# Kernel optimization log

Hardware: AMD Instinct MI355X
Metric: run time of the kernel (lower is better)

Reference implementation:

```python
import jax, jax.numpy as jnp
import numpy as np

B, T, C = 8, 2048, 1024
FFN = 4 * C
EPS = 1e-5


def layer_norm(x, scale, bias):
    mean = jnp.mean(x, axis=-1, keepdims=True)
    var = jnp.mean(jnp.square(x - mean), axis=-1, keepdims=True)
    return (x - mean) * jax.lax.rsqrt(var + EPS) * scale + bias


def token_shift(x):
    # prepend a zero timestep (zero initial state), drop last: x[:, t-1]
    return jnp.pad(x[:, :-1, :], ((0, 0), (1, 0), (0, 0)))


def wkv_scan(k, v, time_first, time_decay):
    # k, v: [B, T, C]. Numerically-stabilized RWKV WKV recurrence (TimeMixCell).
    w = -jnp.exp(time_decay)  # [C]

    def step(carry, kv):
        a, b, p = carry
        kt, vt = kv
        uk = kt + time_first
        q = jnp.maximum(p, uk)
        e1 = jnp.exp(p - q)
        e2 = jnp.exp(uk - q)
        num = e1 * a + e2 * vt
        den = e1 * b + e2
        wkv = jnp.where(den == 0, 0.0, num / jnp.where(den == 0, 1.0, den))
        cw = w + p
        q2 = jnp.maximum(cw, kt)
        f1 = jnp.exp(cw - q2)
        f2 = jnp.exp(kt - q2)
        return (f1 * a + f2 * vt, f1 * b + f2, q2), wkv

    a0 = jnp.zeros((B, C), dtype=k.dtype)
    b0 = jnp.zeros((B, C), dtype=k.dtype)
    p0 = jnp.full((B, C), 1.0 - 1e30, dtype=k.dtype)
    kT = jnp.moveaxis(k, 1, 0)  # [T, B, C]
    vT = jnp.moveaxis(v, 1, 0)
    _, wkvT = jax.lax.scan(step, (a0, b0, p0), (kT, vT))
    return jnp.moveaxis(wkvT, 0, 1)  # [B, T, C]


def setup_inputs() -> dict:
    key = jax.random.key(0)
    ks = jax.random.split(key, 20)
    n = lambda i, shape, s=1.0: jax.random.normal(ks[i], shape, dtype=jnp.float32) * s
    u = lambda i, shape: jax.random.uniform(ks[i], shape, dtype=jnp.float32)
    return {
        'x': n(0, (B, T, C)),
        'ln1_w': 1.0 + n(1, (C,), 0.02), 'ln1_b': n(2, (C,), 0.02),
        'tm_k': u(3, (C,)), 'tm_v': u(4, (C,)), 'tm_r': u(5, (C,)),
        'Wk': n(6, (C, C), 0.02), 'Wv': n(7, (C, C), 0.02), 'Wr': n(8, (C, C), 0.02),
        'time_first': n(9, (C,), 0.1), 'time_decay': n(10, (C,), 0.5),
        'Wo': n(11, (C, C), 0.02),
        'ln2_w': 1.0 + n(12, (C,), 0.02), 'ln2_b': n(13, (C,), 0.02),
        'cm_k': u(14, (C,)), 'cm_r': u(15, (C,)),
        'Wk_ffn': n(16, (C, FFN), 0.02), 'Wv_ffn': n(17, (FFN, C), 0.02),
        'Wr_ffn': n(18, (C, C), 0.02),
    }


def reference(x, ln1_w, ln1_b, tm_k, tm_v, tm_r, Wk, Wv, Wr, time_first,
              time_decay, Wo, ln2_w, ln2_b, cm_k, cm_r, Wk_ffn, Wv_ffn, Wr_ffn):
    # ---- TimeMixFirst ----
    xn = layer_norm(x, ln1_w, ln1_b)
    xs = token_shift(xn)
    kx = xn * tm_k + xs * (1.0 - tm_k)
    vx = xn * tm_v + xs * (1.0 - tm_v)
    rx = xn * tm_r + xs * (1.0 - tm_r)
    r = jax.nn.sigmoid(rx @ Wr)
    k = kx @ Wk
    v = vx @ Wv
    # ---- TimeMixCell (WKV recurrence) ----
    wkv = wkv_scan(k, v, time_first, time_decay)
    # ---- TimeMixLast ----
    att_out = x + (r * wkv) @ Wo
    # ---- ChannelMix ----
    yn = layer_norm(att_out, ln2_w, ln2_b)
    ys = token_shift(yn)
    kx2 = yn * cm_k + ys * (1.0 - cm_k)
    rx2 = yn * cm_r + ys * (1.0 - cm_r)
    r2 = jax.nn.sigmoid(rx2 @ Wr_ffn)
    vv = jnp.square(jax.nn.relu(kx2 @ Wk_ffn))
    return att_out + r2 * (vv @ Wv_ffn)
```

## Files before the change

kernel.cpp:

```cpp
#include <hip/hip_runtime.h>
#include <hip/hip_bf16.h>

#define B_   8
#define T_   2048
#define C_   1024
#define FFN_ 4096
#define M_   (B_ * T_)
#define EPS_ 1e-5f

typedef __bf16 bf16x8 __attribute__((ext_vector_type(8)));
typedef float  f32x4  __attribute__((ext_vector_type(4)));

__device__ __forceinline__ unsigned short f2bf(float f) {
    union { float f; unsigned int u; } c; c.f = f;
    unsigned int u = c.u;
    u += 0x7fffu + ((u >> 16) & 1u);
    return (unsigned short)(u >> 16);
}
__device__ __forceinline__ float bf2f(unsigned short h) {
    union { unsigned int u; float f; } c; c.u = ((unsigned int)h) << 16;
    return c.f;
}

__global__ __launch_bounds__(256) void wconv_t(const float* __restrict__ src,
                                               unsigned short* __restrict__ dst,
                                               int R, int Cc) {
    __shared__ float tile[32][33];
    int tx = threadIdx.x, ty = threadIdx.y;
    int c0 = blockIdx.x * 32;
    int r0 = blockIdx.y * 32;
#pragma unroll
    for (int i = 0; i < 4; ++i)
        tile[ty + i * 8][tx] = src[(size_t)(r0 + ty + i * 8) * Cc + c0 + tx];
    __syncthreads();
#pragma unroll
    for (int i = 0; i < 4; ++i)
        dst[(size_t)(c0 + ty + i * 8) * R + r0 + tx] = f2bf(tile[tx][ty + i * 8]);
}

__device__ __forceinline__ void block_stats(const float4* __restrict__ p4, int tid,
                                            float* red, float& mean, float& rstd) {
    float4 v = p4[tid];
    float s = v.x + v.y + v.z + v.w;
    float q = v.x * v.x + v.y * v.y + v.z * v.z + v.w * v.w;
#pragma unroll
    for (int off = 32; off >= 1; off >>= 1) {
        s += __shfl_down(s, off, 64);
        q += __shfl_down(q, off, 64);
    }
    int lane = tid & 63, wv = tid >> 6;
    if (lane == 0) { red[wv] = s; red[4 + wv] = q; }
    __syncthreads();
    s = red[0] + red[1] + red[2] + red[3];
    q = red[4] + red[5] + red[6] + red[7];
    mean = s * (1.0f / C_);
    float var = q * (1.0f / C_) - mean * mean;
    rstd = rsqrtf(var + EPS_);
    __syncthreads();
}

__global__ __launch_bounds__(256) void mix1_kernel(
    const float* __restrict__ x, const float* __restrict__ lnw, const float* __restrict__ lnb,
    const float* __restrict__ tmk, const float* __restrict__ tmv, const float* __restrict__ tmr,
    unsigned short* __restrict__ kx, unsigned short* __restrict__ vx, unsigned short* __restrict__ rx) {
    __shared__ float red[8];
    int token = blockIdx.x;
    int t = token & (T_ - 1);
    int tid = threadIdx.x;
    bool hp = (t != 0);
    const float4* xt = (const float4*)(x + (size_t)token * C_);
    const float4* xp = (const float4*)(x + (size_t)(hp ? token - 1 : token) * C_);
    float m1, r1, m0 = 0.f, r0 = 0.f;
    block_stats(xt, tid, red, m1, r1);
    if (hp) block_stats(xp, tid, red, m0, r0);

    float4 xv = xt[tid];
    float4 pv = xp[tid];
    float4 w4 = ((const float4*)lnw)[tid];
    float4 b4 = ((const float4*)lnb)[tid];
    float4 k4 = ((const float4*)tmk)[tid];
    float4 v4 = ((const float4*)tmv)[tid];
    float4 q4 = ((const float4*)tmr)[tid];

    ushort4 ko, vo, ro;
    auto mixone = [&](float xe, float pe, float we, float be, float ke, float ve, float re,
                      unsigned short& koe, unsigned short& voe, unsigned short& roe) {
        float xn = (xe - m1) * r1 * we + be;
        float xs = hp ? ((pe - m0) * r0 * we + be) : 0.f;
        koe = f2bf(xs + ke * (xn - xs));
        voe = f2bf(xs + ve * (xn - xs));
        roe = f2bf(xs + re * (xn - xs));
    };
    mixone(xv.x, pv.x, w4.x, b4.x, k4.x, v4.x, q4.x, ko.x, vo.x, ro.x);
    mixone(xv.y, pv.y, w4.y, b4.y, k4.y, v4.y, q4.y, ko.y, vo.y, ro.y);
    mixone(xv.z, pv.z, w4.z, b4.z, k4.z, v4.z, q4.z, ko.z, vo.z, ro.z);
    mixone(xv.w, pv.w, w4.w, b4.w, k4.w, v4.w, q4.w, ko.w, vo.w, ro.w);
    size_t o = (size_t)token * (C_ / 4) + tid;
    ((ushort4*)kx)[o] = ko;
    ((ushort4*)vx)[o] = vo;
    ((ushort4*)rx)[o] = ro;
}

__global__ __launch_bounds__(256) void mix2_kernel(
    const float* __restrict__ att, const float* __restrict__ lnw, const float* __restrict__ lnb,
    const float* __restrict__ cmk, const float* __restrict__ cmr,
    unsigned short* __restrict__ kx, unsigned short* __restrict__ rx) {
    __shared__ float red[8];
    int token = blockIdx.x;
    int t = token & (T_ - 1);
    int tid = threadIdx.x;
    bool hp = (t != 0);
    const float4* xt = (const float4*)(att + (size_t)token * C_);
    const float4* xp = (const float4*)(att + (size_t)(hp ? token - 1 : token) * C_);
    float m1, r1, m0 = 0.f, r0 = 0.f;
    block_stats(xt, tid, red, m1, r1);
    if (hp) block_stats(xp, tid, red, m0, r0);

    float4 xv = xt[tid];
    float4 pv = xp[tid];
    float4 w4 = ((const float4*)lnw)[tid];
    float4 b4 = ((const float4*)lnb)[tid];
    float4 k4 = ((const float4*)cmk)[tid];
    float4 q4 = ((const float4*)cmr)[tid];

    ushort4 ko, ro;
    auto mixone = [&](float xe, float pe, float we, float be, float ke, float re,
                      unsigned short& koe, unsigned short& roe) {
        float xn = (xe - m1) * r1 * we + be;
        float xs = hp ? ((pe - m0) * r0 * we + be) : 0.f;
        koe = f2bf(xs + ke * (xn - xs));
        roe = f2bf(xs + re * (xn - xs));
    };
    mixone(xv.x, pv.x, w4.x, b4.x, k4.x, q4.x, ko.x, ro.x);
    mixone(xv.y, pv.y, w4.y, b4.y, k4.y, q4.y, ko.y, ro.y);
    mixone(xv.z, pv.z, w4.z, b4.z, k4.z, q4.z, ko.z, ro.z);
    mixone(xv.w, pv.w, w4.w, b4.w, k4.w, q4.w, ko.w, ro.w);
    size_t o = (size_t)token * (C_ / 4) + tid;
    ((ushort4*)kx)[o] = ko;
    ((ushort4*)rx)[o] = ro;
}

__global__ __launch_bounds__(64) void wkv_scan_kernel(
    const float* __restrict__ k, const unsigned short* __restrict__ v,
    unsigned short* rv,
    const float* __restrict__ tf, const float* __restrict__ td) {
    int idx = blockIdx.x * 64 + threadIdx.x;
    int b = idx >> 10, c = idx & (C_ - 1);
    float w = -expf(td[c]);
    float u = tf[c];
    size_t base = (size_t)b * T_ * C_ + c;
    float a = 0.f, bb = 0.f, p = -1e30f;

    float kA[8], vA[8], rA[8], kB[8], vB[8], rB[8];
#pragma unroll
    for (int j = 0; j < 8; ++j) {
        size_t o = base + (size_t)j * C_;
        kA[j] = k[o]; vA[j] = bf2f(v[o]); rA[j] = bf2f(rv[o]);
    }

    auto step = [&](float kt, float vt, float rt, int t) {
        float uk = u + kt;
        float qq = fmaxf(p, uk);
        float e1 = __expf(p - qq), e2 = __expf(uk - qq);
        float num = e1 * a + e2 * vt;
        float den = e1 * bb + e2;
        float wkv = (den == 0.f) ? 0.f : num / den;
        rv[base + (size_t)t * C_] = f2bf(rt * wkv);
        float cw = w + p;
        float q2 = fmaxf(cw, kt);
        float f1 = __expf(cw - q2), f2e = __expf(kt - q2);
        a = f1 * a + f2e * vt;
        bb = f1 * bb + f2e;
        p = q2;
    };

    for (int t0 = 0; t0 < T_; t0 += 16) {
#pragma unroll
        for (int j = 0; j < 8; ++j) {
            int t = t0 + 8 + j; if (t > T_ - 1) t = T_ - 1;
            size_t o = base + (size_t)t * C_;
            kB[j] = k[o]; vB[j] = bf2f(v[o]); rB[j] = bf2f(rv[o]);
        }
#pragma unroll
        for (int j = 0; j < 8; ++j) step(kA[j], vA[j], rA[j], t0 + j);
#pragma unroll
        for (int j = 0; j < 8; ++j) {
            int t = t0 + 16 + j; if (t > T_ - 1) t = T_ - 1;
            size_t o = base + (size_t)t * C_;
            kA[j] = k[o]; vA[j] = bf2f(v[o]); rA[j] = bf2f(rv[o]);
        }
#pragma unroll
        for (int j = 0; j < 8; ++j) step(kB[j], vB[j], rB[j], t0 + 8 + j);
    }
}

template<int EPI>
__global__ __launch_bounds__(256) void gemm_bt(
    const unsigned short* __restrict__ A, const unsigned short* __restrict__ Bt,
    float* Cf, unsigned short* Cb,
    const float* __restrict__ e0f, const unsigned short* __restrict__ e0b,
    int M, int N, int K, int ldb) {
    __shared__ unsigned short Als[128 * 32];
    __shared__ unsigned short Bls[128 * 32];
    int tid = threadIdx.x;
    int lane = tid & 63, wv = tid >> 6;
    int wr = wv >> 1, wc = wv & 1;
    int brow = blockIdx.y * 128, bcol = blockIdx.x * 128;

    f32x4 acc[4][4] = {};

    int ar = tid >> 2, ac = (tid & 3) * 8;
    const unsigned short* ga0 = A + (size_t)(brow + ar) * K + ac;
    const unsigned short* ga1 = A + (size_t)(brow + 64 + ar) * K + ac;
    const unsigned short* gb0 = Bt + (size_t)(bcol + ar) * ldb + ac;
    const unsigned short* gb1 = Bt + (size_t)(bcol + 64 + ar) * ldb + ac;
    unsigned short* la0 = Als + (size_t)(wv * 64) * 8;
    unsigned short* la1 = Als + (size_t)((4 + wv) * 64) * 8;
    unsigned short* lb0 = Bls + (size_t)(wv * 64) * 8;
    unsigned short* lb1 = Bls + (size_t)((4 + wv) * 64) * 8;

    int fa = (lane & 15) * 32 + (lane >> 4) * 8;

    for (int kt = 0; kt < K; kt += 32) {
        __builtin_amdgcn_global_load_lds((const __attribute__((address_space(1))) void*)(ga0 + kt),
                                         (__attribute__((address_space(3))) void*)la0, 16, 0, 0);
        __builtin_amdgcn_global_load_lds((const __attribute__((address_space(1))) void*)(ga1 + kt),
                                         (__attribute__((address_space(3))) void*)la1, 16, 0, 0);
        __builtin_amdgcn_global_load_lds((const __attribute__((address_space(1))) void*)(gb0 + kt),
                                         (__attribute__((address_space(3))) void*)lb0, 16, 0, 0);
        __builtin_amdgcn_global_load_lds((const __attribute__((address_space(1))) void*)(gb1 + kt),
                                         (__attribute__((address_space(3))) void*)lb1, 16, 0, 0);
        __syncthreads();
        bf16x8 af[4], bfr[4];
#pragma unroll
        for (int m = 0; m < 4; ++m)
            af[m] = *(const bf16x8*)&Als[(wr * 64 + m * 16) * 32 + fa];
#pragma unroll
        for (int n = 0; n < 4; ++n)
            bfr[n] = *(const bf16x8*)&Bls[(wc * 64 + n * 16) * 32 + fa];
#pragma unroll
        for (int m = 0; m < 4; ++m)
#pragma unroll
            for (int n = 0; n < 4; ++n)
                acc[m][n] = __builtin_amdgcn_mfma_f32_16x16x32_bf16(af[m], bfr[n], acc[m][n], 0, 0, 0);
        __syncthreads();
    }

#pragma unroll
    for (int m = 0; m < 4; ++m) {
#pragma unroll
        for (int n = 0; n < 4; ++n) {
#pragma unroll
            for (int j = 0; j < 4; ++j) {
                int row = brow + wr * 64 + m * 16 + (lane >> 4) * 4 + j;
                int col = bcol + wc * 64 + n * 16 + (lane & 15);
                size_t o = (size_t)row * N + col;
                float val = acc[m][n][j];
                if constexpr (EPI == 0) Cf[o] = val;
                else if constexpr (EPI == 2) Cf[o] = val + e0f[o];
                else if constexpr (EPI == 3) { float tt = fmaxf(val, 0.f); Cb[o] = f2bf(tt * tt); }
                else if constexpr (EPI == 5) Cb[o] = f2bf(1.f / (1.f + __expf(-val)));
                else if constexpr (EPI == 6) Cb[o] = f2bf(val);
                else if constexpr (EPI == 7) Cf[o] = Cf[o] + bf2f(e0b[o]) * val;
            }
        }
    }
}

extern "C" void kernel_launch(void* const* d_in, const int* in_sizes, int n_in,
                              void* d_out, int out_size, void* d_ws, size_t ws_size,
                              hipStream_t stream) {
    const float* x    = (const float*)d_in[0];
    const float* ln1w = (const float*)d_in[1];
    const float* ln1b = (const float*)d_in[2];
    const float* tmk  = (const float*)d_in[3];
    const float* tmv  = (const float*)d_in[4];
    const float* tmr  = (const float*)d_in[5];
    const float* Wk   = (const float*)d_in[6];
    const float* Wv   = (const float*)d_in[7];
    const float* Wr   = (const float*)d_in[8];
    const float* tf   = (const float*)d_in[9];
    const float* td   = (const float*)d_in[10];
    const float* Wo   = (const float*)d_in[11];
    const float* ln2w = (const float*)d_in[12];
    const float* ln2b = (const float*)d_in[13];
    const float* cmk  = (const float*)d_in[14];
    const float* cmr  = (const float*)d_in[15];
    const float* Wkf  = (const float*)d_in[16];
    const float* Wvf  = (const float*)d_in[17];
    const float* Wrf  = (const float*)d_in[18];
    float* out = (float*)d_out;

    char* ws = (char*)d_ws;
    size_t off = 0;
    auto alloc = [&](size_t bytes) {
        char* p = ws + off;
        off += (bytes + 255) & ~(size_t)255;
        return p;
    };
    unsigned short* WkT  = (unsigned short*)alloc((size_t)C_ * C_ * 2);
    unsigned short* WvT  = (unsigned short*)alloc((size_t)C_ * C_ * 2);
    unsigned short* WrT  = (unsigned short*)alloc((size_t)C_ * C_ * 2);
    unsigned short* WoT  = (unsigned short*)alloc((size_t)C_ * C_ * 2);
    unsigned short* WrfT = (unsigned short*)alloc((size_t)C_ * C_ * 2);
    unsigned short* WkfT = (unsigned short*)alloc((size_t)C_ * FFN_ * 2);
    unsigned short* WvfT = (unsigned short*)alloc((size_t)FFN_ * C_ * 2);
    unsigned short* P1 = (unsigned short*)alloc((size_t)M_ * C_ * 2);
    unsigned short* P2 = (unsigned short*)alloc((size_t)M_ * C_ * 2);
    unsigned short* P3 = (unsigned short*)alloc((size_t)M_ * C_ * 2);

    dim3 tb(32, 8);
    wconv_t<<<dim3(C_ / 32, C_ / 32), tb, 0, stream>>>(Wk, WkT, C_, C_);
    wconv_t<<<dim3(C_ / 32, C_ / 32), tb, 0, stream>>>(Wv, WvT, C_, C_);
    wconv_t<<<dim3(C_ / 32, C_ / 32), tb, 0, stream>>>(Wr, WrT, C_, C_);
    wconv_t<<<dim3(C_ / 32, C_ / 32), tb, 0, stream>>>(Wo, WoT, C_, C_);
    wconv_t<<<dim3(C_ / 32, C_ / 32), tb, 0, stream>>>(Wrf, WrfT, C_, C_);
    wconv_t<<<dim3(FFN_ / 32, C_ / 32), tb, 0, stream>>>(Wkf, WkfT, C_, FFN_);
    wconv_t<<<dim3(C_ / 32, FFN_ / 32), tb, 0, stream>>>(Wvf, WvfT, FFN_, C_);

    mix1_kernel<<<M_, 256, 0, stream>>>(x, ln1w, ln1b, tmk, tmv, tmr, P1, P2, P3);

    dim3 gC(C_ / 128, M_ / 128);
    gemm_bt<0><<<gC, 256, 0, stream>>>(P1, WkT, out, nullptr, nullptr, nullptr, M_, C_, C_, C_);
    gemm_bt<6><<<gC, 256, 0, stream>>>(P2, WvT, nullptr, P1, nullptr, nullptr, M_, C_, C_, C_);
    gemm_bt<5><<<gC, 256, 0, stream>>>(P3, WrT, nullptr, P2, nullptr, nullptr, M_, C_, C_, C_);

    wkv_scan_kernel<<<(B_ * C_) / 64, 64, 0, stream>>>(out, P1, P2, tf, td);

    gemm_bt<2><<<gC, 256, 0, stream>>>(P2, WoT, out, nullptr, x, nullptr, M_, C_, C_, C_);

    mix2_kernel<<<M_, 256, 0, stream>>>(out, ln2w, ln2b, cmk, cmr, P1, P3);

    gemm_bt<5><<<gC, 256, 0, stream>>>(P3, WrfT, nullptr, P2, nullptr, nullptr, M_, C_, C_, C_);

    for (int h = 0; h < 4; ++h) {
        gemm_bt<3><<<dim3(1024 / 128, M_ / 128), 256, 0, stream>>>(
            P1, WkfT + (size_t)h * 1024 * C_, nullptr, P3, nullptr, nullptr, M_, 1024, C_, C_);
        gemm_bt<7><<<gC, 256, 0, stream>>>(
            P3, WvfT + (size_t)h * 1024, out, nullptr, nullptr, P2, M_, C_, 1024, FFN_);
    }

    (void)in_sizes; (void)n_in; (void)out_size; (void)ws_size;
}
```

Baseline: 1.471 ms.

## Parallelize WKV scan over time chunks with a three-pass chunked scan

```diff
diff --git a/kernel.cpp b/kernel.cpp
--- a/kernel.cpp
+++ b/kernel.cpp
@@ -7,6 +7,8 @@
 #define FFN_ 4096
 #define M_   (B_ * T_)
 #define EPS_ 1e-5f
+#define NC_  16
+#define LC_  (T_ / NC_)
 
 typedef __bf16 bf16x8 __attribute__((ext_vector_type(8)));
 typedef float  f32x4  __attribute__((ext_vector_type(4)));
@@ -140,16 +142,89 @@
     ((ushort4*)rx)[o] = ro;
 }
 
-__global__ __launch_bounds__(64) void wkv_scan_kernel(
+
+__global__ __launch_bounds__(256) void wkv_pass1(
+    const float* __restrict__ k, const unsigned short* __restrict__ v,
+    const float* __restrict__ td,
+    float* __restrict__ SA, float* __restrict__ SB, float* __restrict__ SP) {
+    int idx = blockIdx.x * 256 + threadIdx.x;
+    int c = idx & (C_ - 1);
+    int b = (idx >> 10) & (B_ - 1);
+    int ch = idx >> 13;
+    float w = -expf(td[c]);
+    size_t base = ((size_t)b * T_ + (size_t)ch * LC_) * C_ + c;
+    float a = 0.f, bb = 0.f, p = -1e30f;
+
+    float kA[8], vA[8], kB[8], vB[8];
+#pragma unroll
+    for (int j = 0; j < 8; ++j) {
+        size_t o = base + (size_t)j * C_;
+        kA[j] = k[o]; vA[j] = bf2f(v[o]);
+    }
+    auto step = [&](float kt, float vt) {
+        float cw = w + p;
+        float q2 = fmaxf(cw, kt);
+        float f1 = __expf(cw - q2), f2e = __expf(kt - q2);
+        a = f1 * a + f2e * vt;
+        bb = f1 * bb + f2e;
+        p = q2;
+    };
+    for (int t0 = 0; t0 < LC_; t0 += 16) {
+#pragma unroll
+        for (int j = 0; j < 8; ++j) {
+            size_t o = base + (size_t)(t0 + 8 + j) * C_;
+            kB[j] = k[o]; vB[j] = bf2f(v[o]);
+        }
+#pragma unroll
+        for (int j = 0; j < 8; ++j) step(kA[j], vA[j]);
+#pragma unroll
+        for (int j = 0; j < 8; ++j) {
+            int tt = t0 + 16 + j; if (tt > LC_ - 1) tt = LC_ - 1;
+            size_t o = base + (size_t)tt * C_;
+            kA[j] = k[o]; vA[j] = bf2f(v[o]);
+        }
+#pragma unroll
+        for (int j = 0; j < 8; ++j) step(kB[j], vB[j]);
+    }
+    SA[idx] = a; SB[idx] = bb; SP[idx] = p;
+}
+
+__global__ __launch_bounds__(256) void wkv_combine(
+    const float* __restrict__ td,
+    const float* __restrict__ SA, const float* __restrict__ SB, const float* __restrict__ SP,
+    float* __restrict__ PA, float* __restrict__ PB, float* __restrict__ PP) {
+    int idx = blockIdx.x * 256 + threadIdx.x;
+    int c = idx & (C_ - 1);
+    float wL = -expf(td[c]) * (float)LC_;
+    float aP = 0.f, bP = 0.f, pP = -1e30f;
+    PA[idx] = aP; PB[idx] = bP; PP[idx] = pP;
+    for (int j = 1; j < NC_; ++j) {
+        int s = (j - 1) * (B_ * C_) + idx;
+        float as = SA[s], bs = SB[s], ps = SP[s];
+        float pd = pP + wL;
+        float q = fmaxf(pd, ps);
+        float e1 = __expf(pd - q), e2 = __expf(ps - q);
+        aP = e1 * aP + e2 * as;
+        bP = e1 * bP + e2 * bs;
+        pP = q;
+        int d = j * (B_ * C_) + idx;
+        PA[d] = aP; PB[d] = bP; PP[d] = pP;
+    }
+}
+
+__global__ __launch_bounds__(256) void wkv_pass2(
     const float* __restrict__ k, const unsigned short* __restrict__ v,
     unsigned short* rv,
-    const float* __restrict__ tf, const float* __restrict__ td) {
-    int idx = blockIdx.x * 64 + threadIdx.x;
-    int b = idx >> 10, c = idx & (C_ - 1);
+    const float* __restrict__ tf, const float* __restrict__ td,
+    const float* __restrict__ PA, const float* __restrict__ PB, const float* __restrict__ PP) {
+    int idx = blockIdx.x * 256 + threadIdx.x;
+    int c = idx & (C_ - 1);
+    int b = (idx >> 10) & (B_ - 1);
+    int ch = idx >> 13;
     float w = -expf(td[c]);
     float u = tf[c];
-    size_t base = (size_t)b * T_ * C_ + c;
-    float a = 0.f, bb = 0.f, p = -1e30f;
+    size_t base = ((size_t)b * T_ + (size_t)ch * LC_) * C_ + c;
+    float a = PA[idx], bb = PB[idx], p = PP[idx];
 
     float kA[8], vA[8], rA[8], kB[8], vB[8], rB[8];
 #pragma unroll
@@ -157,7 +232,6 @@
         size_t o = base + (size_t)j * C_;
         kA[j] = k[o]; vA[j] = bf2f(v[o]); rA[j] = bf2f(rv[o]);
     }
-
     auto step = [&](float kt, float vt, float rt, int t) {
         float uk = u + kt;
         float qq = fmaxf(p, uk);
@@ -173,20 +247,18 @@
         bb = f1 * bb + f2e;
         p = q2;
     };
-
-    for (int t0 = 0; t0 < T_; t0 += 16) {
+    for (int t0 = 0; t0 < LC_; t0 += 16) {
 #pragma unroll
         for (int j = 0; j < 8; ++j) {
-            int t = t0 + 8 + j; if (t > T_ - 1) t = T_ - 1;
-            size_t o = base + (size_t)t * C_;
+            size_t o = base + (size_t)(t0 + 8 + j) * C_;
             kB[j] = k[o]; vB[j] = bf2f(v[o]); rB[j] = bf2f(rv[o]);
         }
 #pragma unroll
         for (int j = 0; j < 8; ++j) step(kA[j], vA[j], rA[j], t0 + j);
 #pragma unroll
         for (int j = 0; j < 8; ++j) {
-            int t = t0 + 16 + j; if (t > T_ - 1) t = T_ - 1;
-            size_t o = base + (size_t)t * C_;
+            int tt = t0 + 16 + j; if (tt > LC_ - 1) tt = LC_ - 1;
+            size_t o = base + (size_t)tt * C_;
             kA[j] = k[o]; vA[j] = bf2f(v[o]); rA[j] = bf2f(rv[o]);
         }
 #pragma unroll
@@ -308,6 +380,12 @@
     unsigned short* P1 = (unsigned short*)alloc((size_t)M_ * C_ * 2);
     unsigned short* P2 = (unsigned short*)alloc((size_t)M_ * C_ * 2);
     unsigned short* P3 = (unsigned short*)alloc((size_t)M_ * C_ * 2);
+    float* SA = (float*)alloc((size_t)NC_ * B_ * C_ * 4);
+    float* SB = (float*)alloc((size_t)NC_ * B_ * C_ * 4);
+    float* SP = (float*)alloc((size_t)NC_ * B_ * C_ * 4);
+    float* PA = (float*)alloc((size_t)NC_ * B_ * C_ * 4);
+    float* PBp = (float*)alloc((size_t)NC_ * B_ * C_ * 4);
+    float* PP = (float*)alloc((size_t)NC_ * B_ * C_ * 4);
 
     dim3 tb(32, 8);
     wconv_t<<<dim3(C_ / 32, C_ / 32), tb, 0, stream>>>(Wk, WkT, C_, C_);
@@ -325,7 +403,9 @@
     gemm_bt<6><<<gC, 256, 0, stream>>>(P2, WvT, nullptr, P1, nullptr, nullptr, M_, C_, C_, C_);
     gemm_bt<5><<<gC, 256, 0, stream>>>(P3, WrT, nullptr, P2, nullptr, nullptr, M_, C_, C_, C_);
 
-    wkv_scan_kernel<<<(B_ * C_) / 64, 64, 0, stream>>>(out, P1, P2, tf, td);
+    wkv_pass1<<<(B_ * C_ * (NC_ - 1)) / 256, 256, 0, stream>>>(out, P1, td, SA, SB, SP);
+    wkv_combine<<<(B_ * C_) / 256, 256, 0, stream>>>(td, SA, SB, SP, PA, PBp, PP);
+    wkv_pass2<<<(B_ * C_ * NC_) / 256, 256, 0, stream>>>(out, P1, P2, tf, td, PA, PBp, PP);
 
     gemm_bt<2><<<gC, 256, 0, stream>>>(P2, WoT, out, nullptr, x, nullptr, M_, C_, C_, C_);
 
```

Result: faster. 1.259 ms (-14.4%).
